# Kernel tuning notes

Measured on AMD Instinct MI355X. Metric: run time of the kernel, lower is better.

Reference implementation:

```python
import jax, jax.numpy as jnp
import numpy as np

NL, NH, H, FF, V, P = 12, 12, 768, 3072, 30522, 512
B, L, S = 4, 512, 8
DH = H // NH


def _layer_norm(x, g, b, eps=1e-12):
    m = x.mean(-1, keepdims=True)
    v = jnp.mean((x - m) ** 2, axis=-1, keepdims=True)
    return (x - m) * jax.lax.rsqrt(v + eps) * g + b


def setup_inputs() -> dict:
    key = jax.random.key(0)
    ks = iter(jax.random.split(key, 40))
    pm = lambda shape: jax.random.normal(next(ks), shape, jnp.float32) * 0.02
    inp = {
        'word_emb': pm((V, H)), 'pos_emb': pm((P, H)), 'type_emb': pm((2, H)),
        'emb_ln_g': jnp.ones((H,), jnp.float32), 'emb_ln_b': jnp.zeros((H,), jnp.float32),
        'Wq': pm((NL, H, H)), 'bq': jnp.zeros((NL, H), jnp.float32),
        'Wk': pm((NL, H, H)), 'bk': jnp.zeros((NL, H), jnp.float32),
        'Wv': pm((NL, H, H)), 'bv': jnp.zeros((NL, H), jnp.float32),
        'Wo': pm((NL, H, H)), 'bo': jnp.zeros((NL, H), jnp.float32),
        'attn_ln_g': jnp.ones((NL, H), jnp.float32), 'attn_ln_b': jnp.zeros((NL, H), jnp.float32),
        'W1': pm((NL, H, FF)), 'b1': jnp.zeros((NL, FF), jnp.float32),
        'W2': pm((NL, FF, H)), 'b2': jnp.zeros((NL, H), jnp.float32),
        'ffn_ln_g': jnp.ones((NL, H), jnp.float32), 'ffn_ln_b': jnp.zeros((NL, H), jnp.float32),
        'fc_w': pm((H,)), 'fc_b': jnp.zeros((), jnp.float32),
    }
    inp['input_ids'] = jax.random.randint(next(ks), (B, L), 0, V)
    inp['token_type_ids'] = jnp.zeros((B, L), jnp.int32)
    # valid-length prefix attention_mask and sorted bos_locations (history = 64)
    vl = np.array([384 + 16 * (i % 8) for i in range(B)])
    hist = 64
    am = (np.arange(L)[None, :] < vl[:, None]).astype(np.int32)
    bos = np.stack([hist + (np.arange(S) * (v - hist)) // S for v in vl]).astype(np.int64)
    inp['attention_mask'] = jnp.asarray(am)
    inp['bos_locations'] = jnp.asarray(bos)
    return inp


def _forward(word_emb, pos_emb, type_emb, emb_ln_g, emb_ln_b,
             Wq, bq, Wk, bk, Wv, bv, Wo, bo, attn_ln_g, attn_ln_b,
             W1, b1, W2, b2, ffn_ln_g, ffn_ln_b, fc_w, fc_b,
             input_ids, token_type_ids, attention_mask, bos_locations):
    Bs, Ls = input_ids.shape
    t = jnp.arange(Ls)
    valid_len = attention_mask.sum(-1)                       # [B]
    hist = bos_locations[:, 0]                               # [B] history length
    # segment id per token: number of bos positions <= t, minus 1 (-1 in history)
    seg = (bos_locations[:, :, None] <= t[None, None, :]).sum(1) - 1   # [B,L]
    valid = t[None, :] < valid_len[:, None]                  # [B,L]
    # block-diagonal candidate attention mask (history rows/cols fully visible)
    p = t[None, :, None]
    q = t[None, None, :]
    hist_pq = (p < hist[:, None, None]) | (q < hist[:, None, None])
    same_seg = seg[:, :, None] == seg[:, None, :]
    mask = valid[:, :, None] & valid[:, None, :] & (hist_pq | same_seg)  # [B,L,L]
    bias = jnp.where(mask, 0.0, -10000.0).astype(jnp.float32)[:, None, :, :]  # [B,1,L,L]

    # BERT embeddings
    x = word_emb[input_ids] + pos_emb[t][None] + type_emb[token_type_ids]
    x = _layer_norm(x, emb_ln_g, emb_ln_b)
    scale = 1.0 / jnp.sqrt(jnp.asarray(DH, x.dtype))

    for l in range(NL):
        qh = (x @ Wq[l] + bq[l]).reshape(Bs, Ls, NH, DH)
        kh = (x @ Wk[l] + bk[l]).reshape(Bs, Ls, NH, DH)
        vh = (x @ Wv[l] + bv[l]).reshape(Bs, Ls, NH, DH)
        scores = jnp.einsum('bqhd,bkhd->bhqk', qh, kh) * scale + bias
        probs = jax.nn.softmax(scores, axis=-1)
        ctx = jnp.einsum('bhqk,bkhd->bqhd', probs, vh).reshape(Bs, Ls, H)
        x = _layer_norm(x + ctx @ Wo[l] + bo[l], attn_ln_g[l], attn_ln_b[l])
        h = jax.nn.gelu(x @ W1[l] + b1[l], approximate=False)
        x = _layer_norm(x + h @ W2[l] + b2[l], ffn_ln_g[l], ffn_ln_b[l])

    # variable-length segment mean pooling via membership matmul
    starts = bos_locations                                   # [B,S]
    ends = jnp.concatenate([bos_locations[:, 1:], valid_len[:, None]], axis=1)
    memb = ((t[None, None, :] >= starts[:, :, None]) &
            (t[None, None, :] < ends[:, :, None])).astype(x.dtype)        # [B,S,L]
    pooled = jnp.einsum('bsl,bld->bsd', memb, x) / memb.sum(-1, keepdims=True)
    logits = pooled @ fc_w + fc_b                            # [B,S]
    return jnp.squeeze(logits)


def reference(word_emb, pos_emb, type_emb, emb_ln_g, emb_ln_b,
              Wq, bq, Wk, bk, Wv, bv, Wo, bo, attn_ln_g, attn_ln_b,
              W1, b1, W2, b2, ffn_ln_g, ffn_ln_b, fc_w, fc_b,
              input_ids, token_type_ids, attention_mask, bos_locations):
    return _forward(word_emb, pos_emb, type_emb, emb_ln_g, emb_ln_b,
                    Wq, bq, Wk, bk, Wv, bv, Wo, bo, attn_ln_g, attn_ln_b,
                    W1, b1, W2, b2, ffn_ln_g, ffn_ln_b, fc_w, fc_b,
                    input_ids, token_type_ids, attention_mask, bos_locations)
```

## Files before the change

kernel.cpp:

```cpp
#include <hip/hip_runtime.h>
#include <math.h>

#define HH 768
#define FF 3072
#define NL 12
#define NH 12
#define DH 64
#define BB 4
#define LL 512
#define SS 8
#define MM (BB*LL)
#define WQSZ (HH*HH)
#define W1SZ (HH*FF)
#define LWB 7077888
#define OFF_WO 1769472
#define OFF_W1 2359296
#define OFF_W2 4718592

typedef short bf16x8 __attribute__((ext_vector_type(8)));
typedef float f32x4 __attribute__((ext_vector_type(4)));

__device__ inline ushort f2b(float f) {
  unsigned u = __float_as_uint(f);
  unsigned r = (u + 0x7FFFu + ((u >> 16) & 1u)) >> 16;
  return (ushort)r;
}

__global__ void prep_kernel(const int* __restrict__ am, const int* __restrict__ bos,
                            int* __restrict__ seg, int* __restrict__ vl) {
  int b = blockIdx.x;
  int t = threadIdx.x;
  __shared__ int red[512];
  red[t] = am[b*LL + t];
  __syncthreads();
  for (int off = 256; off > 0; off >>= 1) {
    if (t < off) red[t] += red[t+off];
    __syncthreads();
  }
  if (t == 0) vl[b] = red[0];
  int cnt = 0;
  #pragma unroll
  for (int s = 0; s < SS; s++) cnt += (bos[b*SS + s] <= t) ? 1 : 0;
  seg[b*LL + t] = cnt - 1;
}

__global__ __launch_bounds__(256) void embed_ln_kernel(
    const float* __restrict__ word_emb, const float* __restrict__ pos_emb,
    const float* __restrict__ type_emb, const float* __restrict__ g,
    const float* __restrict__ bta, const int* __restrict__ ids,
    const int* __restrict__ tts, float* __restrict__ x, ushort* __restrict__ xb)
{
  int row = blockIdx.x;
  int l = row & (LL-1);
  int t = threadIdx.x;
  int id = ids[row];
  int ty = tts[row];
  float v[3];
  float s = 0.f, sq = 0.f;
  #pragma unroll
  for (int j = 0; j < 3; j++) {
    int c = t + j*256;
    float val = word_emb[(size_t)id*HH + c] + pos_emb[l*HH + c] + type_emb[ty*HH + c];
    v[j] = val; s += val; sq += val*val;
  }
  __shared__ float rs[256], rq[256];
  rs[t] = s; rq[t] = sq;
  __syncthreads();
  for (int off = 128; off > 0; off >>= 1) {
    if (t < off) { rs[t] += rs[t+off]; rq[t] += rq[t+off]; }
    __syncthreads();
  }
  float mean = rs[0] / HH;
  float var  = rq[0] / HH - mean*mean;
  float inv  = rsqrtf(var + 1e-12f);
  #pragma unroll
  for (int j = 0; j < 3; j++) {
    int c = t + j*256;
    float o = (v[j]-mean)*inv*g[c] + bta[c];
    x[(size_t)row*HH + c] = o;
    xb[(size_t)row*HH + c] = f2b(o);
  }
}

__global__ __launch_bounds__(256) void add_ln2_kernel(
    const float* __restrict__ xin, const float* __restrict__ y1,
    const float* __restrict__ y2, const float* __restrict__ g,
    const float* __restrict__ bta, float* __restrict__ xout, ushort* __restrict__ xb)
{
  int row = blockIdx.x;
  int t = threadIdx.x;
  float v[3];
  float s = 0.f, sq = 0.f;
  #pragma unroll
  for (int j = 0; j < 3; j++) {
    int c = t + j*256;
    size_t ix = (size_t)row*HH + c;
    float val = xin[ix] + y1[ix] + y2[ix];
    v[j] = val; s += val; sq += val*val;
  }
  __shared__ float rs[256], rq[256];
  rs[t] = s; rq[t] = sq;
  __syncthreads();
  for (int off = 128; off > 0; off >>= 1) {
    if (t < off) { rs[t] += rs[t+off]; rq[t] += rq[t+off]; }
    __syncthreads();
  }
  float mean = rs[0] / HH;
  float var  = rq[0] / HH - mean*mean;
  float inv  = rsqrtf(var + 1e-12f);
  #pragma unroll
  for (int j = 0; j < 3; j++) {
    int c = t + j*256;
    float o = (v[j]-mean)*inv*g[c] + bta[c];
    xout[(size_t)row*HH + c] = o;
    xb[(size_t)row*HH + c] = f2b(o);
  }
}

__global__ __launch_bounds__(256) void convw_all_kernel(
    const float* __restrict__ Wq, const float* __restrict__ Wk,
    const float* __restrict__ Wv, const float* __restrict__ Wo,
    const float* __restrict__ W1, const float* __restrict__ W2,
    ushort* __restrict__ wbuf)
{
  int idx = blockIdx.x;
  int l = idx / 1728;
  int t0 = idx % 1728;
  size_t base = (size_t)l * LWB;
  const float* src; ushort* dst; int Nsrc, dstK, k0, n0src, n0dst;
  if (t0 < 432) {
    int nt = t0 / 12, kt = t0 % 12;
    int z = nt / 12, ntl = nt % 12;
    src = (z == 0 ? Wq : z == 1 ? Wk : Wv) + (size_t)l*WQSZ;
    dst = wbuf + base;
    Nsrc = HH; dstK = HH; k0 = kt*64; n0src = ntl*64; n0dst = nt*64;
  } else if (t0 < 576) {
    int t = t0 - 432; int nt = t / 12, kt = t % 12;
    src = Wo + (size_t)l*WQSZ;
    dst = wbuf + base + OFF_WO;
    Nsrc = HH; dstK = HH; k0 = kt*64; n0src = n0dst = nt*64;
  } else if (t0 < 1152) {
    int t = t0 - 576; int nt = t / 12, kt = t % 12;
    src = W1 + (size_t)l*W1SZ;
    dst = wbuf + base + OFF_W1;
    Nsrc = FF; dstK = HH; k0 = kt*64; n0src = n0dst = nt*64;
  } else {
    int t = t0 - 1152; int nt = t / 48, kt = t % 48;
    src = W2 + (size_t)l*W1SZ;
    dst = wbuf + base + OFF_W2;
    Nsrc = HH; dstK = FF; k0 = kt*64; n0src = n0dst = nt*64;
  }
  __shared__ ushort tt[64][72];
  int tid = threadIdx.x;
  int r = tid >> 4, c = (tid & 15) << 2;
  #pragma unroll
  for (int i = 0; i < 4; i++) {
    int rr = r + i*16;
    float4 v = *(const float4*)&src[(size_t)(k0+rr)*Nsrc + n0src + c];
    tt[c+0][rr] = f2b(v.x); tt[c+1][rr] = f2b(v.y);
    tt[c+2][rr] = f2b(v.z); tt[c+3][rr] = f2b(v.w);
  }
  __syncthreads();
  #pragma unroll
  for (int it = 0; it < 2; it++) {
    int n = it*32 + (tid >> 3);
    int k = (tid & 7) << 3;
    ushort tmp8[8];
    #pragma unroll
    for (int j = 0; j < 8; j++) tmp8[j] = tt[n][k+j];
    *(uint4*)&dst[(size_t)(n0dst+n)*dstK + k0 + k] = *(const uint4*)tmp8;
  }
}

template<int MODE>
__global__ __launch_bounds__(256) void gemm_bt(
    const ushort* __restrict__ A, const ushort* __restrict__ Bt,
    const float* __restrict__ ba, const float* __restrict__ bb,
    const float* __restrict__ bc, float* __restrict__ Cf,
    ushort* __restrict__ Cb, int M, int N, int K)
{
  __shared__ __align__(16) ushort As[2][128*32];
  __shared__ __align__(16) ushort Bs[2][64*32];
  const int tid = threadIdx.x;
  const int lane = tid & 63, wid = tid >> 6;
  const int wm = wid >> 1, wn = wid & 1;
  const int m0 = blockIdx.y * 128, n0 = blockIdx.x * 64;
  int kbeg = 0, NT = K >> 5;
  if (MODE == 2) { int kh = K >> 1; kbeg = blockIdx.z * kh; NT = kh >> 5; }

  auto STAGE = [&](int buf, int k0) {
    #pragma unroll
    for (int j = 0; j < 2; j++) {
      int c = j*256 + tid;
      int r = c >> 2;
      int kk = ((c & 3) ^ (r & 3)) << 3;
      __builtin_amdgcn_global_load_lds(
        (const __attribute__((address_space(1))) void*)(A + (size_t)(m0+r)*K + k0 + kk),
        (__attribute__((address_space(3))) void*)(&As[buf][c*8]), 16, 0, 0);
    }
    {
      int c = tid;
      int r = c >> 2;
      int kk = ((c & 3) ^ (r & 3)) << 3;
      __builtin_amdgcn_global_load_lds(
        (const __attribute__((address_space(1))) void*)(Bt + (size_t)(n0+r)*K + k0 + kk),
        (__attribute__((address_space(3))) void*)(&Bs[buf][c*8]), 16, 0, 0);
    }
  };

  f32x4 acc[4][2] = {};
  STAGE(0, kbeg);
  __syncthreads();
  int cur = 0;
  for (int t = 0; t < NT; ++t) {
    if (t + 1 < NT) STAGE(cur ^ 1, kbeg + (t+1)*32);
    bf16x8 af[4], bf[2];
    #pragma unroll
    for (int mi = 0; mi < 4; mi++) {
      int r = wm*64 + mi*16 + (lane & 15);
      int slot = (lane >> 4) ^ (r & 3);
      af[mi] = *(const bf16x8*)(&As[cur][r*32 + slot*8]);
    }
    #pragma unroll
    for (int ni = 0; ni < 2; ni++) {
      int r = wn*32 + ni*16 + (lane & 15);
      int slot = (lane >> 4) ^ (r & 3);
      bf[ni] = *(const bf16x8*)(&Bs[cur][r*32 + slot*8]);
    }
    #pragma unroll
    for (int mi = 0; mi < 4; mi++)
      #pragma unroll
      for (int ni = 0; ni < 2; ni++)
        acc[mi][ni] = __builtin_amdgcn_mfma_f32_16x16x32_bf16(af[mi], bf[ni], acc[mi][ni], 0, 0, 0);
    __syncthreads();
    cur ^= 1;
  }

  #pragma unroll
  for (int mi = 0; mi < 4; mi++) {
    #pragma unroll
    for (int ni = 0; ni < 2; ni++) {
      int col = n0 + wn*32 + ni*16 + (lane & 15);
      if (MODE == 0) {
        int z = (col >= 1536) ? 2 : (col >= 768 ? 1 : 0);
        int cc = col - z*768;
        float bvv = (z == 0 ? ba : z == 1 ? bb : bc)[cc];
        #pragma unroll
        for (int r = 0; r < 4; r++) {
          int row = m0 + wm*64 + mi*16 + (lane >> 4)*4 + r;
          Cb[(size_t)z*MM*HH + (size_t)row*HH + cc] = f2b(acc[mi][ni][r] + bvv);
        }
      } else if (MODE == 1) {
        float bvv = ba[col];
        #pragma unroll
        for (int r = 0; r < 4; r++) {
          int row = m0 + wm*64 + mi*16 + (lane >> 4)*4 + r;
          float v = acc[mi][ni][r] + bvv;
          v = 0.5f * v * (1.0f + erff(v * 0.70710678118654752f));
          Cb[(size_t)row*N + col] = f2b(v);
        }
      } else {
        float bvv = (blockIdx.z == 0) ? ba[col] : 0.f;
        #pragma unroll
        for (int r = 0; r < 4; r++) {
          int row = m0 + wm*64 + mi*16 + (lane >> 4)*4 + r;
          Cf[(size_t)blockIdx.z*M*N + (size_t)row*N + col] = acc[mi][ni][r] + bvv;
        }
      }
    }
  }
}

__global__ __launch_bounds__(256) void attn_mfma_kernel(
    const ushort* __restrict__ Q, const ushort* __restrict__ Kp, const ushort* __restrict__ Vp,
    ushort* __restrict__ ctx, const int* __restrict__ seg, const int* __restrict__ vl,
    const int* __restrict__ bos)
{
  const int q0 = blockIdx.x * 64;
  const int h  = blockIdx.y;
  const int b  = blockIdx.z;
  const int tid = threadIdx.x;
  const int lane = tid & 63;
  const int wid = tid >> 6;

  __shared__ __align__(16) char Ks[8192];
  __shared__ __align__(16) char Vt[8192];
  __shared__ __align__(16) char Ps[4][2048];
  __shared__ int segk[64];

  const int qrow_frag = q0 + wid*16 + (lane & 15);
  bf16x8 qf[2];
  #pragma unroll
  for (int c = 0; c < 2; c++)
    qf[c] = *(const bf16x8*)&Q[((size_t)(b*LL + qrow_frag))*HH + h*DH + 32*c + (lane >> 4)*8];

  const int vlb  = vl[b];
  const int hist = bos[b*SS];
  int segq[4]; bool qvalid[4], qhist[4];
  #pragma unroll
  for (int r = 0; r < 4; r++) {
    int qg = q0 + wid*16 + (lane >> 4)*4 + r;
    segq[r]   = seg[b*LL + qg];
    qvalid[r] = qg < vlb;
    qhist[r]  = qg < hist;
  }

  float mrow[4], lrow[4];
  #pragma unroll
  for (int r = 0; r < 4; r++) { mrow[r] = -1e30f; lrow[r] = 0.f; }
  f32x4 Oacc[4] = {};

  for (int k0 = 0; k0 < LL; k0 += 64) {
    __syncthreads();
    #pragma unroll
    for (int p = 0; p < 2; p++) {
      int r  = (tid >> 3) + 32*p;
      int c8 = (tid & 7) * 8;
      uint4 kv = *(const uint4*)&Kp[((size_t)(b*LL + k0 + r))*HH + h*DH + c8];
      *(uint4*)(Ks + (r*128 + ((c8*2) ^ ((r & 7) << 4)))) = kv;
    }
    #pragma unroll
    for (int p = 0; p < 2; p++) {
      int k  = lane;
      int d0 = wid*8 + 32*p;
      uint4 vv = *(const uint4*)&Vp[((size_t)(b*LL + k0 + k))*HH + h*DH + d0];
      const ushort* pv = (const ushort*)&vv;
      #pragma unroll
      for (int j = 0; j < 8; j++) {
        int d = d0 + j;
        *(ushort*)(Vt + (d*128 + ((k*2) ^ ((d & 7) << 4)))) = pv[j];
      }
    }
    if (tid < 64) segk[tid] = seg[b*LL + k0 + tid];
    __syncthreads();

    f32x4 sacc[4] = {};
    #pragma unroll
    for (int t = 0; t < 4; t++) {
      int krow = (lane & 15) + 16*t;
      #pragma unroll
      for (int c = 0; c < 2; c++) {
        bf16x8 kf = *(const bf16x8*)(Ks + (krow*128 +
                      (((32*c + (lane >> 4)*8)*2) ^ ((krow & 7) << 4))));
        sacc[t] = __builtin_amdgcn_mfma_f32_16x16x32_bf16(qf[c], kf, sacc[t], 0, 0, 0);
      }
    }

    #pragma unroll
    for (int t = 0; t < 4; t++) {
      int kg = k0 + (lane & 15) + 16*t;
      bool kvalid = kg < vlb;
      bool khist  = kg < hist;
      int  sk     = segk[(lane & 15) + 16*t];
      #pragma unroll
      for (int r = 0; r < 4; r++) {
        bool ok = qvalid[r] && kvalid && (khist || qhist[r] || (segq[r] == sk));
        sacc[t][r] = sacc[t][r]*0.125f + (ok ? 0.f : -10000.f);
      }
    }

    float scl[4];
    #pragma unroll
    for (int r = 0; r < 4; r++) {
      float rm = fmaxf(fmaxf(sacc[0][r], sacc[1][r]), fmaxf(sacc[2][r], sacc[3][r]));
      rm = fmaxf(rm, __shfl_xor(rm, 1));
      rm = fmaxf(rm, __shfl_xor(rm, 2));
      rm = fmaxf(rm, __shfl_xor(rm, 4));
      rm = fmaxf(rm, __shfl_xor(rm, 8));
      float mnew = fmaxf(mrow[r], rm);
      scl[r] = __expf(mrow[r] - mnew);
      float rsum = 0.f;
      #pragma unroll
      for (int t = 0; t < 4; t++) {
        float p = __expf(sacc[t][r] - mnew);
        sacc[t][r] = p;
        rsum += p;
      }
      rsum += __shfl_xor(rsum, 1);
      rsum += __shfl_xor(rsum, 2);
      rsum += __shfl_xor(rsum, 4);
      rsum += __shfl_xor(rsum, 8);
      mrow[r] = mnew;
      lrow[r] = lrow[r]*scl[r] + rsum;
    }

    char* Pl = Ps[wid];
    #pragma unroll
    for (int t = 0; t < 4; t++) {
      #pragma unroll
      for (int r = 0; r < 4; r++) {
        int q = (lane >> 4)*4 + r;
        int k = (lane & 15) + 16*t;
        *(ushort*)(Pl + (q*128 + ((k*2) ^ ((q & 7) << 4)))) = f2b(sacc[t][r]);
      }
    }
    asm volatile("s_waitcnt lgkmcnt(0)" ::: "memory");
    bf16x8 pf[2];
    #pragma unroll
    for (int c = 0; c < 2; c++) {
      int q = lane & 15;
      int k = 32*c + (lane >> 4)*8;
      pf[c] = *(const bf16x8*)(Pl + (q*128 + ((k*2) ^ ((q & 7) << 4))));
    }

    #pragma unroll
    for (int nt = 0; nt < 4; nt++) {
      #pragma unroll
      for (int r = 0; r < 4; r++) Oacc[nt][r] *= scl[r];
      int d = (lane & 15) + 16*nt;
      #pragma unroll
      for (int c = 0; c < 2; c++) {
        int k = 32*c + (lane >> 4)*8;
        bf16x8 vf = *(const bf16x8*)(Vt + (d*128 + ((k*2) ^ ((d & 7) << 4))));
        Oacc[nt] = __builtin_amdgcn_mfma_f32_16x16x32_bf16(pf[c], vf, Oacc[nt], 0, 0, 0);
      }
    }
  }

  #pragma unroll
  for (int nt = 0; nt < 4; nt++) {
    #pragma unroll
    for (int r = 0; r < 4; r++) {
      int q = q0 + wid*16 + (lane >> 4)*4 + r;
      int d = h*DH + (lane & 15) + 16*nt;
      ctx[(size_t)(b*LL + q)*HH + d] = f2b(Oacc[nt][r] / lrow[r]);
    }
  }
}

__global__ __launch_bounds__(256) void rowdot_kernel(const float* __restrict__ x,
                                                     const float* __restrict__ w,
                                                     float* __restrict__ rd) {
  int row = blockIdx.x;
  int t = threadIdx.x;
  float s = 0.f;
  #pragma unroll
  for (int j = 0; j < 3; j++) {
    int c = t + j*256;
    s = fmaf(x[(size_t)row*HH + c], w[c], s);
  }
  __shared__ float red[256];
  red[t] = s;
  __syncthreads();
  for (int off = 128; off > 0; off >>= 1) {
    if (t < off) red[t] += red[t+off];
    __syncthreads();
  }
  if (t == 0) rd[row] = red[0];
}

__global__ void logits_kernel(const float* __restrict__ rd, const int* __restrict__ bos,
                              const int* __restrict__ vl, const float* __restrict__ fcb,
                              float* __restrict__ out) {
  int i = threadIdx.x;
  if (i >= BB*SS) return;
  int b = i / SS, s = i % SS;
  int start = bos[b*SS + s];
  int end   = (s == SS-1) ? vl[b] : bos[b*SS + s + 1];
  float sum = 0.f;
  for (int t = start; t < end; t++) sum += rd[b*LL + t];
  out[i] = sum / (float)(end - start) + fcb[0];
}

extern "C" void kernel_launch(void* const* d_in, const int* in_sizes, int n_in,
                              void* d_out, int out_size, void* d_ws, size_t ws_size,
                              hipStream_t stream) {
  const float* word_emb  = (const float*)d_in[0];
  const float* pos_emb   = (const float*)d_in[1];
  const float* type_emb  = (const float*)d_in[2];
  const float* emb_ln_g  = (const float*)d_in[3];
  const float* emb_ln_b  = (const float*)d_in[4];
  const float* Wq        = (const float*)d_in[5];
  const float* bq        = (const float*)d_in[6];
  const float* Wk        = (const float*)d_in[7];
  const float* bk        = (const float*)d_in[8];
  const float* Wv        = (const float*)d_in[9];
  const float* bv        = (const float*)d_in[10];
  const float* Wo        = (const float*)d_in[11];
  const float* bo        = (const float*)d_in[12];
  const float* attn_ln_g = (const float*)d_in[13];
  const float* attn_ln_b = (const float*)d_in[14];
  const float* W1        = (const float*)d_in[15];
  const float* b1        = (const float*)d_in[16];
  const float* W2        = (const float*)d_in[17];
  const float* b2        = (const float*)d_in[18];
  const float* ffn_ln_g  = (const float*)d_in[19];
  const float* ffn_ln_b  = (const float*)d_in[20];
  const float* fc_w      = (const float*)d_in[21];
  const float* fc_b      = (const float*)d_in[22];
  const int* input_ids   = (const int*)d_in[23];
  const int* token_type  = (const int*)d_in[24];
  const int* am          = (const int*)d_in[25];
  const int* bos         = (const int*)d_in[26];
  float* out = (float*)d_out;

  char* w = (char*)d_ws;
  float*  x       = (float*)w;  w += (size_t)MM*HH*4;
  float*  tmp     = (float*)w;  w += (size_t)2*MM*HH*4;
  ushort* qkv_bf  = (ushort*)w; w += (size_t)3*MM*HH*2;
  ushort* x_bf    = (ushort*)w; w += (size_t)MM*HH*2;
  ushort* ctx_bf  = (ushort*)w; w += (size_t)MM*HH*2;
  ushort* hbuf_bf = (ushort*)w; w += (size_t)MM*FF*2;
  ushort* wbuf    = (ushort*)w; w += (size_t)NL*LWB*2;
  float*  rd      = (float*)w;  w += (size_t)MM*4;
  int*    seg     = (int*)w;    w += (size_t)MM*4;
  int*    vl      = (int*)w;    w += 64;

  prep_kernel<<<BB, 512, 0, stream>>>(am, bos, seg, vl);
  convw_all_kernel<<<NL*1728, 256, 0, stream>>>(Wq, Wk, Wv, Wo, W1, W2, wbuf);
  embed_ln_kernel<<<MM, 256, 0, stream>>>(word_emb, pos_emb, type_emb,
                                          emb_ln_g, emb_ln_b, input_ids, token_type, x, x_bf);

  dim3 gqkv(2304/64, MM/128);
  dim3 g_ff1(FF/64, MM/128);
  dim3 g_sk(HH/64, MM/128, 2);
  dim3 gattn(LL/64, NH, BB);

  for (int l = 0; l < NL; l++) {
    const ushort* Wqkv_t = wbuf + (size_t)l*LWB;
    const ushort* Wo_t   = wbuf + (size_t)l*LWB + OFF_WO;
    const ushort* W1_t   = wbuf + (size_t)l*LWB + OFF_W1;
    const ushort* W2_t   = wbuf + (size_t)l*LWB + OFF_W2;

    gemm_bt<0><<<gqkv, 256, 0, stream>>>(x_bf, Wqkv_t,
        bq + (size_t)l*HH, bk + (size_t)l*HH, bv + (size_t)l*HH,
        nullptr, qkv_bf, MM, 2304, HH);

    attn_mfma_kernel<<<gattn, 256, 0, stream>>>(qkv_bf, qkv_bf + (size_t)MM*HH,
                                                qkv_bf + (size_t)2*MM*HH, ctx_bf, seg, vl, bos);

    gemm_bt<2><<<g_sk, 256, 0, stream>>>(ctx_bf, Wo_t,
        bo + (size_t)l*HH, nullptr, nullptr, tmp, nullptr, MM, HH, HH);

    add_ln2_kernel<<<MM, 256, 0, stream>>>(x, tmp, tmp + (size_t)MM*HH,
                                           attn_ln_g + (size_t)l*HH,
                                           attn_ln_b + (size_t)l*HH, x, x_bf);

    gemm_bt<1><<<g_ff1, 256, 0, stream>>>(x_bf, W1_t,
        b1 + (size_t)l*FF, nullptr, nullptr, nullptr, hbuf_bf, MM, FF, HH);

    gemm_bt<2><<<g_sk, 256, 0, stream>>>(hbuf_bf, W2_t,
        b2 + (size_t)l*HH, nullptr, nullptr, tmp, nullptr, MM, HH, FF);

    add_ln2_kernel<<<MM, 256, 0, stream>>>(x, tmp, tmp + (size_t)MM*HH,
                                           ffn_ln_g + (size_t)l*HH,
                                           ffn_ln_b + (size_t)l*HH, x, x_bf);
  }

  rowdot_kernel<<<MM, 256, 0, stream>>>(x, fc_w, rd);
  logits_kernel<<<1, 64, 0, stream>>>(rd, bos, vl, fc_b, out);
}
```

Baseline: 1.645 ms.

## Deepen GEMM K-tile to 64, swizzle blocks across XCDs, split-K by four

The bf16 MFMA GEMM now stages 64-wide K tiles, which doubles LDS use, and uses an 8-way XOR swizzle so there are half as many barriers per unit of work. Block indices are remapped so that contiguous tiles land on the same XCD, aiming for better L2 reuse. The split-K GEMMs for Wo and W2 go from 2 to 4 partitions for more parallelism, and the add+LayerNorm kernel is templated to sum four partial buffers. The cost is more partial-sum traffic and a larger temp workspace.

```diff
diff --git a/kernel.cpp b/kernel.cpp
--- a/kernel.cpp
+++ b/kernel.cpp
@@ -26,6 +26,16 @@
   return (ushort)r;
 }
 
+__device__ inline void swz_xy(int& x, int& y) {
+  int gx = gridDim.x, gy = gridDim.y;
+  int flat = blockIdx.x + blockIdx.y * gx;
+  int nwg = gx * gy;
+  int q = nwg >> 3, r = nwg & 7;
+  int xcd = flat & 7, off = flat >> 3;
+  int wgid = (xcd < r ? xcd * (q + 1) : r * (q + 1) + (xcd - r) * q) + off;
+  x = wgid / gy; y = wgid - x * gy;
+}
+
 __global__ void prep_kernel(const int* __restrict__ am, const int* __restrict__ bos,
                             int* __restrict__ seg, int* __restrict__ vl) {
   int b = blockIdx.x;
@@ -82,10 +92,11 @@
   }
 }
 
-__global__ __launch_bounds__(256) void add_ln2_kernel(
-    const float* __restrict__ xin, const float* __restrict__ y1,
-    const float* __restrict__ y2, const float* __restrict__ g,
-    const float* __restrict__ bta, float* __restrict__ xout, ushort* __restrict__ xb)
+template<int NP>
+__global__ __launch_bounds__(256) void add_ln_kernel(
+    const float* __restrict__ xin, const float* __restrict__ y,
+    const float* __restrict__ g, const float* __restrict__ bta,
+    float* __restrict__ xout, ushort* __restrict__ xb)
 {
   int row = blockIdx.x;
   int t = threadIdx.x;
@@ -95,7 +106,9 @@
   for (int j = 0; j < 3; j++) {
     int c = t + j*256;
     size_t ix = (size_t)row*HH + c;
-    float val = xin[ix] + y1[ix] + y2[ix];
+    float val = xin[ix];
+    #pragma unroll
+    for (int p = 0; p < NP; p++) val += y[(size_t)p*MM*HH + ix];
     v[j] = val; s += val; sq += val*val;
   }
   __shared__ float rs[256], rq[256];
@@ -179,29 +192,32 @@
     const float* __restrict__ bc, float* __restrict__ Cf,
     ushort* __restrict__ Cb, int M, int N, int K)
 {
-  __shared__ __align__(16) ushort As[2][128*32];
-  __shared__ __align__(16) ushort Bs[2][64*32];
+  __shared__ __align__(16) ushort As[2][128*64];
+  __shared__ __align__(16) ushort Bs[2][64*64];
   const int tid = threadIdx.x;
   const int lane = tid & 63, wid = tid >> 6;
   const int wm = wid >> 1, wn = wid & 1;
-  const int m0 = blockIdx.y * 128, n0 = blockIdx.x * 64;
-  int kbeg = 0, NT = K >> 5;
-  if (MODE == 2) { int kh = K >> 1; kbeg = blockIdx.z * kh; NT = kh >> 5; }
+  int bx, by; swz_xy(bx, by);
+  const int m0 = by * 128, n0 = bx * 64;
+  int kbeg = 0, kcnt = K;
+  if (MODE == 2) { kcnt = K >> 2; kbeg = blockIdx.z * kcnt; }
+  const int NT = kcnt >> 6;
 
   auto STAGE = [&](int buf, int k0) {
     #pragma unroll
-    for (int j = 0; j < 2; j++) {
+    for (int j = 0; j < 4; j++) {
       int c = j*256 + tid;
-      int r = c >> 2;
-      int kk = ((c & 3) ^ (r & 3)) << 3;
+      int r = c >> 3;
+      int kk = ((c & 7) ^ (r & 7)) << 3;
       __builtin_amdgcn_global_load_lds(
         (const __attribute__((address_space(1))) void*)(A + (size_t)(m0+r)*K + k0 + kk),
         (__attribute__((address_space(3))) void*)(&As[buf][c*8]), 16, 0, 0);
     }
-    {
-      int c = tid;
-      int r = c >> 2;
-      int kk = ((c & 3) ^ (r & 3)) << 3;
+    #pragma unroll
+    for (int j = 0; j < 2; j++) {
+      int c = j*256 + tid;
+      int r = c >> 3;
+      int kk = ((c & 7) ^ (r & 7)) << 3;
       __builtin_amdgcn_global_load_lds(
         (const __attribute__((address_space(1))) void*)(Bt + (size_t)(n0+r)*K + k0 + kk),
         (__attribute__((address_space(3))) void*)(&Bs[buf][c*8]), 16, 0, 0);
@@ -213,25 +229,33 @@
   __syncthreads();
   int cur = 0;
   for (int t = 0; t < NT; ++t) {
-    if (t + 1 < NT) STAGE(cur ^ 1, kbeg + (t+1)*32);
-    bf16x8 af[4], bf[2];
+    if (t + 1 < NT) STAGE(cur ^ 1, kbeg + (t+1)*64);
+    bf16x8 af[4][2], bfv[2][2];
     #pragma unroll
     for (int mi = 0; mi < 4; mi++) {
-      int r = wm*64 + mi*16 + (lane & 15);
-      int slot = (lane >> 4) ^ (r & 3);
-      af[mi] = *(const bf16x8*)(&As[cur][r*32 + slot*8]);
+      int row = wm*64 + mi*16 + (lane & 15);
+      #pragma unroll
+      for (int ks = 0; ks < 2; ks++) {
+        int kb = (ks*64 + ((lane >> 4) << 4)) ^ ((row & 7) << 4);
+        af[mi][ks] = *(const bf16x8*)((const char*)&As[cur][0] + row*128 + kb);
+      }
     }
     #pragma unroll
     for (int ni = 0; ni < 2; ni++) {
-      int r = wn*32 + ni*16 + (lane & 15);
-      int slot = (lane >> 4) ^ (r & 3);
-      bf[ni] = *(const bf16x8*)(&Bs[cur][r*32 + slot*8]);
-    }
-    #pragma unroll
-    for (int mi = 0; mi < 4; mi++)
-      #pragma unroll
-      for (int ni = 0; ni < 2; ni++)
-        acc[mi][ni] = __builtin_amdgcn_mfma_f32_16x16x32_bf16(af[mi], bf[ni], acc[mi][ni], 0, 0, 0);
+      int row = wn*32 + ni*16 + (lane & 15);
+      #pragma unroll
+      for (int ks = 0; ks < 2; ks++) {
+        int kb = (ks*64 + ((lane >> 4) << 4)) ^ ((row & 7) << 4);
+        bfv[ni][ks] = *(const bf16x8*)((const char*)&Bs[cur][0] + row*128 + kb);
+      }
+    }
+    #pragma unroll
+    for (int ks = 0; ks < 2; ks++)
+      #pragma unroll
+      for (int mi = 0; mi < 4; mi++)
+        #pragma unroll
+        for (int ni = 0; ni < 2; ni++)
+          acc[mi][ni] = __builtin_amdgcn_mfma_f32_16x16x32_bf16(af[mi][ks], bfv[ni][ks], acc[mi][ni], 0, 0, 0);
     __syncthreads();
     cur ^= 1;
   }
@@ -242,7 +266,7 @@
     for (int ni = 0; ni < 2; ni++) {
       int col = n0 + wn*32 + ni*16 + (lane & 15);
       if (MODE == 0) {
-        int z = (col >= 1536) ? 2 : (col >= 768 ? 1 : 0);
+        int z = n0 / 768;
         int cc = col - z*768;
         float bvv = (z == 0 ? ba : z == 1 ? bb : bc)[cc];
         #pragma unroll
@@ -496,7 +520,7 @@
 
   char* w = (char*)d_ws;
   float*  x       = (float*)w;  w += (size_t)MM*HH*4;
-  float*  tmp     = (float*)w;  w += (size_t)2*MM*HH*4;
+  float*  tmp     = (float*)w;  w += (size_t)4*MM*HH*4;
   ushort* qkv_bf  = (ushort*)w; w += (size_t)3*MM*HH*2;
   ushort* x_bf    = (ushort*)w; w += (size_t)MM*HH*2;
   ushort* ctx_bf  = (ushort*)w; w += (size_t)MM*HH*2;
@@ -513,7 +537,7 @@
 
   dim3 gqkv(2304/64, MM/128);
   dim3 g_ff1(FF/64, MM/128);
-  dim3 g_sk(HH/64, MM/128, 2);
+  dim3 g_sk(HH/64, MM/128, 4);
   dim3 gattn(LL/64, NH, BB);
 
   for (int l = 0; l < NL; l++) {
@@ -532,9 +556,8 @@
     gemm_bt<2><<<g_sk, 256, 0, stream>>>(ctx_bf, Wo_t,
         bo + (size_t)l*HH, nullptr, nullptr, tmp, nullptr, MM, HH, HH);
 
-    add_ln2_kernel<<<MM, 256, 0, stream>>>(x, tmp, tmp + (size_t)MM*HH,
-                                           attn_ln_g + (size_t)l*HH,
-                                           attn_ln_b + (size_t)l*HH, x, x_bf);
+    add_ln_kernel<4><<<MM, 256, 0, stream>>>(x, tmp, attn_ln_g + (size_t)l*HH,
+                                             attn_ln_b + (size_t)l*HH, x, x_bf);
 
     gemm_bt<1><<<g_ff1, 256, 0, stream>>>(x_bf, W1_t,
         b1 + (size_t)l*FF, nullptr, nullptr, nullptr, hbuf_bf, MM, FF, HH);
@@ -542,9 +565,8 @@
     gemm_bt<2><<<g_sk, 256, 0, stream>>>(hbuf_bf, W2_t,
         b2 + (size_t)l*HH, nullptr, nullptr, tmp, nullptr, MM, HH, FF);
 
-    add_ln2_kernel<<<MM, 256, 0, stream>>>(x, tmp, tmp + (size_t)MM*HH,
-                                           ffn_ln_g + (size_t)l*HH,
-                                           ffn_ln_b + (size_t)l*HH, x, x_bf);
+    add_ln_kernel<4><<<MM, 256, 0, stream>>>(x, tmp, ffn_ln_g + (size_t)l*HH,
+                                             ffn_ln_b + (size_t)l*HH, x, x_bf);
   }
 
   rowdot_kernel<<<MM, 256, 0, stream>>>(x, fc_w, rd);
```

Result: faster. 1.460 ms (-11.3%).
